# Kernel tuning notes

Hardware: AMD Instinct MI355X
Metric: run time of the kernel (lower is better)

Reference implementation:

```python
import jax, jax.numpy as jnp
import numpy as np

DIM = 1024
NUM_HEADS = 16
HEAD_DIM = DIM // NUM_HEADS
B, S, E = 4, 8192, 2000


def setup_inputs() -> dict:
    key = jax.random.key(0)
    ks = jax.random.split(key, 16)
    sd = 0.02
    inp = {
        "x": jax.random.normal(ks[0], (B, S, DIM), dtype=jnp.float32),
        "src_indices": jax.random.randint(ks[1], (E,), 0, S),
        "dst_indices": jax.random.randint(ks[2], (E,), 0, S),
        # linear weights stored [in, out] (applied as x @ W + b)
        "Wq": jax.random.normal(ks[3], (DIM, DIM), jnp.float32) * sd,
        "bq": jnp.zeros((DIM,), jnp.float32),
        "Wk": jax.random.normal(ks[4], (DIM, DIM), jnp.float32) * sd,
        "bk": jnp.zeros((DIM,), jnp.float32),
        "Wv": jax.random.normal(ks[5], (DIM, DIM), jnp.float32) * sd,
        "bv": jnp.zeros((DIM,), jnp.float32),
        "Wo": jax.random.normal(ks[6], (DIM, DIM), jnp.float32) * sd,
        "bo": jnp.zeros((DIM,), jnp.float32),
        "edge_weight": jax.random.normal(ks[7], (1, NUM_HEADS, 1), jnp.float32),
        "W1": jax.random.normal(ks[8], (2 * HEAD_DIM, HEAD_DIM), jnp.float32) * sd,
        "b1": jnp.zeros((HEAD_DIM,), jnp.float32),
        "W2": jax.random.normal(ks[9], (HEAD_DIM, 1), jnp.float32) * sd,
        "b2": jnp.zeros((1,), jnp.float32),
    }
    return inp


def reference(x, src_indices, dst_indices, Wq, bq, Wk, bk, Wv, bv, Wo, bo,
              edge_weight, W1, b1, W2, b2):
    Bs, Sl, D = x.shape
    H, hd = NUM_HEADS, HEAD_DIM
    scale = hd ** -0.5

    def heads(t):  # [B,S,D] -> [B,H,S,hd]
        return t.reshape(Bs, Sl, H, hd).transpose(0, 2, 1, 3)

    q = heads(x @ Wq + bq)
    k = heads(x @ Wk + bk)
    v = heads(x @ Wv + bv)

    q_src = jnp.take(q, src_indices, axis=2)   # [B,H,E,hd]
    k_dst = jnp.take(k, dst_indices, axis=2)   # [B,H,E,hd]
    v_dst = jnp.take(v, dst_indices, axis=2)   # [B,H,E,hd]

    ef = jnp.concatenate([q_src, k_dst], axis=-1)          # [B,H,E,2hd]
    h = jax.nn.gelu(ef @ W1 + b1, approximate=False)       # [B,H,E,hd]
    scores = (h @ W2 + b2) * scale                         # [B,H,E,1]
    attn = jax.nn.softmax(scores, axis=2)                  # softmax over all edges
    attn = attn * edge_weight[..., None]                   # [1,H,1,1] broadcast

    weighted = attn * v_dst                                # [B,H,E,hd]
    out = jnp.zeros((Bs, H, Sl, hd), x.dtype).at[:, :, src_indices, :].add(weighted)

    final = out.transpose(0, 2, 1, 3).reshape(Bs, Sl, D)
    return final @ Wo + bo
```

## Files before the change

kernel.cpp:

```cpp
#include <hip/hip_runtime.h>
#include <hip/hip_bf16.h>
#include <math.h>

#define DIMK 1024
#define NH 16
#define HD 64
#define BB 4
#define SS 8192
#define NKT 32

typedef __attribute__((ext_vector_type(8))) short bf16x8;
typedef __attribute__((ext_vector_type(8))) unsigned short ushort8;
typedef __attribute__((ext_vector_type(4))) unsigned short us4;
typedef __attribute__((ext_vector_type(4))) float f32x4;

#define MFMA16(a, b, c) __builtin_amdgcn_mfma_f32_16x16x32_bf16((a), (b), (c), 0, 0, 0)

__device__ __forceinline__ unsigned short f32_to_bf16_rne(float f) {
  unsigned int u = __float_as_uint(f);
  u = (u + 0x7fffu + ((u >> 16) & 1u)) >> 16;
  return (unsigned short)u;
}
__device__ __forceinline__ float bf16_bits_to_f32(unsigned short b) {
  return __uint_as_float(((unsigned int)b) << 16);
}
__device__ __forceinline__ void gload16(const void* g, void* l) {
  __builtin_amdgcn_global_load_lds((const __attribute__((address_space(1))) void*)g,
                                   (__attribute__((address_space(3))) void*)l, 16, 0, 0);
}

__global__ __launch_bounds__(256) void fill_out_kernel(const float4* __restrict__ bo4,
                                                       float4* __restrict__ out, int total4) {
  for (int i = blockIdx.x * 256 + threadIdx.x; i < total4; i += gridDim.x * 256)
    out[i] = bo4[i & 255];
}

__global__ __launch_bounds__(256) void prep_w2(
    const float* __restrict__ Wv, const float* __restrict__ Wo,
    unsigned short* __restrict__ Bkv, unsigned short* __restrict__ Bo) {
  const float* W = blockIdx.z ? Wo : Wv;
  unsigned short* Bpan = blockIdx.z ? Bo : Bkv;
  const int pnoff = blockIdx.z ? 0 : 8;
  __shared__ float st[64][65];
  const int bk = blockIdx.x * 64, bn = blockIdx.y * 64;
  const int t = threadIdx.x;
  const int lr = t >> 4, lc = (t & 15) * 4;
#pragma unroll
  for (int i = 0; i < 4; i++) {
    int k = lr + i * 16;
    float4 v = *(const float4*)(W + (size_t)(bk + k) * DIMK + bn + lc);
    st[k][lc] = v.x; st[k][lc + 1] = v.y; st[k][lc + 2] = v.z; st[k][lc + 3] = v.w;
  }
  __syncthreads();
  const int ktile = (bk + lc) >> 5, c = lc & 31;
#pragma unroll
  for (int i = 0; i < 4; i++) {
    const int nl = lr + i * 16;
    const int n = bn + nl;
    const int r = n & 127, pn = (n >> 7) + pnoff;
    const int q = (c >> 3) ^ ((r >> 1) & 3);
    const size_t byteoff = (size_t)r * 64 + q * 16 + (c & 7) * 2;
    us4 hv, lv;
#pragma unroll
    for (int j = 0; j < 4; j++) {
      float v = st[lc + j][nl];
      unsigned short hb = f32_to_bf16_rne(v);
      hv[j] = hb;
      lv[j] = f32_to_bf16_rne(v - bf16_bits_to_f32(hb));
    }
    char* base = (char*)Bpan;
    *(us4*)(base + (((size_t)pn * 64 + ktile) << 13) + byteoff) = hv;
    *(us4*)(base + (((size_t)pn * 64 + 32 + ktile) << 13) + byteoff) = lv;
  }
}

__global__ __launch_bounds__(256) void prep_wfold(
    const float* __restrict__ Wq, const float* __restrict__ Wk,
    const float* __restrict__ W1,
    unsigned short* __restrict__ Bq, unsigned short* __restrict__ Bkv) {
  const int which = blockIdx.z;
  const float* W = which ? Wk : Wq;
  unsigned short* Bpan = which ? Bkv : Bq;
  const int d_off = which ? 64 : 0;
  const int cc = blockIdx.x, jc = blockIdx.y;
  __shared__ float Wb[64][65];
  __shared__ float W1b[64][65];
  const int t = threadIdx.x;
  for (int idx = t; idx < 64 * 64; idx += 256) {
    int rrow = idx >> 6, dd = idx & 63;
    Wb[rrow][dd] = W[(size_t)(cc * 64 + rrow) * DIMK + jc * 64 + dd];
    W1b[rrow][dd] = W1[(size_t)(d_off + rrow) * 64 + dd];
  }
  __syncthreads();
  const int n = t & 63, g0 = t >> 6;
  const int pn = jc >> 1;
  const int r = (jc & 1) * 64 + n;
  const int sw = (r >> 1) & 3;
  char* base = (char*)Bpan;
#pragma unroll
  for (int i = 0; i < 4; ++i) {
    const int cl0 = (g0 + 4 * i) * 4;
    float a0 = 0.f, a1 = 0.f, a2 = 0.f, a3 = 0.f;
    for (int d = 0; d < 64; ++d) {
      const float w1v = W1b[d][n];
      a0 = fmaf(Wb[cl0 + 0][d], w1v, a0);
      a1 = fmaf(Wb[cl0 + 1][d], w1v, a1);
      a2 = fmaf(Wb[cl0 + 2][d], w1v, a2);
      a3 = fmaf(Wb[cl0 + 3][d], w1v, a3);
    }
    float av[4] = {a0, a1, a2, a3};
    const int c = cc * 64 + cl0;
    const int kt = c >> 5, kcol = c & 31;
    const int q = (kcol >> 3) ^ sw;
    const size_t byteoff = (size_t)r * 64 + q * 16 + (kcol & 7) * 2;
    us4 hv, lv;
#pragma unroll
    for (int j = 0; j < 4; j++) {
      unsigned short hb = f32_to_bf16_rne(av[j]);
      hv[j] = hb;
      lv[j] = f32_to_bf16_rne(av[j] - bf16_bits_to_f32(hb));
    }
    *(us4*)(base + (((size_t)pn * 64 + kt) << 13) + byteoff) = hv;
    *(us4*)(base + (((size_t)pn * 64 + 32 + kt) << 13) + byteoff) = lv;
  }
}

__global__ __launch_bounds__(256) void prep_bias(
    const float* __restrict__ bq, const float* __restrict__ bk,
    const float* __restrict__ b1, const float* __restrict__ W1,
    float* __restrict__ bqf, float* __restrict__ bkf) {
  const int j = blockIdx.x * 256 + threadIdx.x;
  const int h = j >> 6, n = j & 63;
  float sq = 0.f, sk = 0.f;
  for (int d = 0; d < 64; ++d) {
    sq = fmaf(bq[h * 64 + d], W1[d * 64 + n], sq);
    sk = fmaf(bk[h * 64 + d], W1[(64 + d) * 64 + n], sk);
  }
  bqf[j] = sq;
  bkf[j] = sk + b1[n];
}

__global__ __launch_bounds__(256) void prep_a(const float* __restrict__ X,
                                              const int* __restrict__ gidx,
                                              unsigned short* __restrict__ Apan, int M, int E) {
  const int row = blockIdx.x;
  const int r = row & 255, mt = row >> 8;
  const int c0 = threadIdx.x * 4;
  const int kt = c0 >> 5, c = c0 & 31;
  const int q = (c >> 3) ^ ((r >> 1) & 3);
  const size_t byteoff = (size_t)r * 64 + q * 16 + (c & 7) * 2;
  char* base = (char*)Apan;
  us4 hv = (us4){0, 0, 0, 0}, lv = (us4){0, 0, 0, 0};
  if (row < M) {
    const float* sr;
    if (gidx) {
      int b = row / E, e = row - b * E;
      sr = X + ((size_t)b * SS + gidx[e]) * DIMK;
    } else {
      sr = X + (size_t)row * DIMK;
    }
    float4 v = *(const float4*)(sr + c0);
    float vv[4] = {v.x, v.y, v.z, v.w};
#pragma unroll
    for (int i = 0; i < 4; i++) {
      unsigned short hb = f32_to_bf16_rne(vv[i]);
      hv[i] = hb;
      lv[i] = f32_to_bf16_rne(vv[i] - bf16_bits_to_f32(hb));
    }
  }
  *(us4*)(base + (((size_t)(mt * 64 + kt)) << 14) + byteoff) = hv;
  *(us4*)(base + (((size_t)(mt * 64 + 32 + kt)) << 14) + byteoff) = lv;
}

__global__ __launch_bounds__(1024) void first_occ(const int* __restrict__ src,
                                                  int* __restrict__ fidx,
                                                  int* __restrict__ mark, int E) {
  __shared__ int tbl[SS];
  for (int i = threadIdx.x; i < SS; i += 1024) tbl[i] = 0x7fffffff;
  __syncthreads();
  for (int e = threadIdx.x; e < E; e += 1024) atomicMin(&tbl[src[e]], e);
  __syncthreads();
  for (int e = threadIdx.x; e < E; e += 1024) mark[e] = 0;
  __syncthreads();
  for (int e = threadIdx.x; e < E; e += 1024) {
    int f = tbl[src[e]];
    fidx[e] = f;
    if (f != e) mark[f] = 1;
  }
}

template <int BM, int MODE>
__global__ __launch_bounds__(512, 2) void gemmT(
    const unsigned short* __restrict__ Apan, const unsigned short* __restrict__ Bpan,
    const float* __restrict__ bias, const float* __restrict__ bias2,
    float* __restrict__ out, int ldc, int nty,
    const int* __restrict__ fidx, const int* __restrict__ srci, int M, int E) {
  constexpr int MF = BM / 32;
  constexpr int NF = 4;
  constexpr int AT = BM * 32;
  __shared__ unsigned short ldsAh[2][AT];
  __shared__ unsigned short ldsAl[2][AT];
  __shared__ unsigned short ldsBh[2][8192];
  __shared__ unsigned short ldsBl[2][8192];

  const int tid = threadIdx.x, lane = tid & 63, wv = tid >> 6;
  const int wr = wv >> 2, wc = wv & 3;

  const int w = (blockIdx.x & 7) * ((int)gridDim.x >> 3) + ((int)blockIdx.x >> 3);
  const int mi = w / nty, nt_ = w - mi * nty;
  const int m0 = mi * BM, n0 = nt_ * 256;

  const int rr = lane & 15, lq = lane >> 4;
  const int swz = (rr >> 1) & 3;
  const int aoff = (wr * (BM / 2) + rr) * 32 + ((lq ^ swz) << 3);
  const int boff = (wc * 64 + rr) * 32 + ((lq ^ swz) << 3);

  const int pt = (BM == 256) ? mi : (mi >> 1);
  const int rowbase = (BM == 256) ? 0 : (mi & 1) * 128;
  const char* Apb = (const char*)Apan + (((size_t)pt * 64) << 14) + (size_t)rowbase * 64;
  const char* Bpb = (const char*)Bpan;
  const int stoff = wv * 1024 + lane * 16;

  f32x4 acc[MF][NF];
#pragma unroll
  for (int i = 0; i < MF; i++)
#pragma unroll
    for (int j = 0; j < NF; j++) acc[i][j] = (f32x4){0.f, 0.f, 0.f, 0.f};

  auto stage = [&](int kt, int buf) {
    const char* sAh = Apb + ((size_t)kt << 14) + stoff;
    const char* sAl = Apb + ((size_t)(32 + kt) << 14) + stoff;
    gload16(sAh, &ldsAh[buf][wv * 512]);
    gload16(sAl, &ldsAl[buf][wv * 512]);
    if (BM == 256) {
      gload16(sAh + 8192, &ldsAh[buf][wv * 512 + 4096]);
      gload16(sAl + 8192, &ldsAl[buf][wv * 512 + 4096]);
    }
    const char* sB0h = Bpb + (((size_t)(2 * nt_) * 64 + kt) << 13) + stoff;
    const char* sB1h = Bpb + (((size_t)(2 * nt_ + 1) * 64 + kt) << 13) + stoff;
    const char* sB0l = Bpb + (((size_t)(2 * nt_) * 64 + 32 + kt) << 13) + stoff;
    const char* sB1l = Bpb + (((size_t)(2 * nt_ + 1) * 64 + 32 + kt) << 13) + stoff;
    gload16(sB0h, &ldsBh[buf][wv * 512]);
    gload16(sB1h, &ldsBh[buf][wv * 512 + 4096]);
    gload16(sB0l, &ldsBl[buf][wv * 512]);
    gload16(sB1l, &ldsBl[buf][wv * 512 + 4096]);
  };

  stage(0, 0);
  asm volatile("s_waitcnt vmcnt(0)" ::: "memory");
  __builtin_amdgcn_sched_barrier(0);
  __builtin_amdgcn_s_barrier();

  for (int kt = 0; kt < NKT; ++kt) {
    const int buf = kt & 1;
    const unsigned short* Ah = ldsAh[buf];
    const unsigned short* Al = ldsAl[buf];
    const unsigned short* Bh = ldsBh[buf];
    const unsigned short* Bl = ldsBl[buf];

    bf16x8 fbh[NF], fah[MF], fal[MF], fbl[NF];
#pragma unroll
    for (int nf = 0; nf < NF; ++nf) fbh[nf] = *(const bf16x8*)(Bh + boff + nf * 512);
#pragma unroll
    for (int mf = 0; mf < MF; ++mf) fah[mf] = *(const bf16x8*)(Ah + aoff + mf * 512);
    __builtin_amdgcn_sched_barrier(0);
#pragma unroll
    for (int mf = 0; mf < MF; ++mf) fal[mf] = *(const bf16x8*)(Al + aoff + mf * 512);
    __builtin_amdgcn_sched_barrier(0);
#pragma unroll
    for (int nf = 0; nf < NF; ++nf) fbl[nf] = *(const bf16x8*)(Bl + boff + nf * 512);
    __builtin_amdgcn_sched_barrier(0);

    if (kt + 1 < NKT) stage(kt + 1, buf ^ 1);

    asm volatile("s_waitcnt lgkmcnt(%0)" ::"i"(MF + NF) : "memory");
    __builtin_amdgcn_sched_barrier(0);
    __builtin_amdgcn_s_setprio(1);
#pragma unroll
    for (int mf = 0; mf < MF; ++mf)
#pragma unroll
      for (int nf = 0; nf < NF; ++nf) acc[mf][nf] = MFMA16(fah[mf], fbh[nf], acc[mf][nf]);
    __builtin_amdgcn_s_setprio(0);

    asm volatile("s_waitcnt lgkmcnt(%0)" ::"i"(NF) : "memory");
    __builtin_amdgcn_sched_barrier(0);
    __builtin_amdgcn_s_setprio(1);
#pragma unroll
    for (int mf = 0; mf < MF; ++mf)
#pragma unroll
      for (int nf = 0; nf < NF; ++nf) acc[mf][nf] = MFMA16(fal[mf], fbh[nf], acc[mf][nf]);
    __builtin_amdgcn_s_setprio(0);

    asm volatile("s_waitcnt lgkmcnt(0)" ::: "memory");
    if (kt + 1 < NKT) {
      asm volatile("s_waitcnt vmcnt(0)" ::: "memory");
      __builtin_amdgcn_sched_barrier(0);
      __builtin_amdgcn_s_barrier();
    } else {
      __builtin_amdgcn_sched_barrier(0);
    }

    __builtin_amdgcn_s_setprio(1);
#pragma unroll
    for (int mf = 0; mf < MF; ++mf)
#pragma unroll
      for (int nf = 0; nf < NF; ++nf) acc[mf][nf] = MFMA16(fah[mf], fbl[nf], acc[mf][nf]);
    __builtin_amdgcn_s_setprio(0);
  }

  const int cq = lane >> 4, cr = lane & 15;
#pragma unroll
  for (int nf = 0; nf < NF; ++nf) {
    const int col = n0 + wc * 64 + nf * 16 + cr;
    const float bv = (MODE == 0 && bias2 != nullptr && col >= DIMK) ? bias2[col - DIMK]
                                                                    : bias[col & (DIMK - 1)];
#pragma unroll
    for (int mf = 0; mf < MF; ++mf) {
#pragma unroll
      for (int r = 0; r < 4; ++r) {
        const int mrow = m0 + wr * (BM / 2) + mf * 16 + cq * 4 + r;
        if (mrow >= M) continue;
        if (MODE == 0) {
          out[(size_t)mrow * ldc + col] = acc[mf][nf][r] + bv;
        } else {
          int b = mrow / E, e = mrow - b * E;
          if (fidx[e] == e) {
            int orow = b * SS + srci[e];
            out[(size_t)orow * ldc + col] = acc[mf][nf][r] + bv;
          }
        }
      }
    }
  }
}

__global__ __launch_bounds__(256) void edge_scores_f(
    const float* __restrict__ hq, const float* __restrict__ hk,
    const float* __restrict__ W2, const float* __restrict__ b2,
    float* __restrict__ scores, int E, int CH) {
  const int tid = threadIdx.x, lane = tid & 63, w = tid >> 6;
  const int bh = blockIdx.x / CH, ch = blockIdx.x - bh * CH;
  const int b = bh >> 4, h = bh & 15;
  const float w2 = W2[lane];
  const float b2v = b2[0];
#pragma unroll
  for (int i = 0; i < 8; ++i) {
    const int e = ch * 32 + w * 8 + i;
    if (e >= E) break;
    const size_t row = (size_t)(b * E + e);
    float hv = hq[row * 1024 + h * 64 + lane] + hk[row * 2048 + h * 64 + lane];
    hv = 0.5f * hv * (1.f + erff(hv * 0.70710678118654752f));
    float p = hv * w2;
#pragma unroll
    for (int off = 32; off; off >>= 1) p += __shfl_xor(p, off, 64);
    if (lane == 0) scores[(size_t)(b * NH + h) * E + e] = (p + b2v) * 0.125f;
  }
}

__global__ __launch_bounds__(256) void softmax_ew(float* __restrict__ scores,
                                                  const float* __restrict__ ew, int E) {
  const int row = blockIdx.x;
  const int h = row & (NH - 1);
  float* s = scores + (size_t)row * E;
  const int tid = threadIdx.x, lane = tid & 63, w = tid >> 6;
  __shared__ float red[4];

  float vals[8];
  float mx = -1e30f;
#pragma unroll
  for (int i = 0; i < 8; i++) {
    int j = tid + i * 256;
    vals[i] = (j < E) ? s[j] : -1e30f;
    mx = fmaxf(mx, vals[i]);
  }
#pragma unroll
  for (int off = 32; off; off >>= 1) mx = fmaxf(mx, __shfl_xor(mx, off, 64));
  if (lane == 0) red[w] = mx;
  __syncthreads();
  mx = fmaxf(fmaxf(red[0], red[1]), fmaxf(red[2], red[3]));
  __syncthreads();

  float sum = 0.f;
#pragma unroll
  for (int i = 0; i < 8; i++) {
    vals[i] = __expf(vals[i] - mx);
    if (tid + i * 256 < E) sum += vals[i];
  }
#pragma unroll
  for (int off = 32; off; off >>= 1) sum += __shfl_xor(sum, off, 64);
  if (lane == 0) red[w] = sum;
  __syncthreads();
  sum = red[0] + red[1] + red[2] + red[3];

  const float scaleout = ew[h] / sum;
#pragma unroll
  for (int i = 0; i < 8; i++) {
    int j = tid + i * 256;
    if (j < E) s[j] = vals[i] * scaleout;
  }
}

__global__ __launch_bounds__(256) void weight_split(
    const float* __restrict__ vd, int ldv, const float* __restrict__ attn,
    float* __restrict__ wrow, unsigned short* __restrict__ Apan, int M, int E) {
  const int row = blockIdx.x;
  const int r = row & 255, mt = row >> 8;
  const int c0 = threadIdx.x * 4;
  const int kt = c0 >> 5, c = c0 & 31;
  const int q = (c >> 3) ^ ((r >> 1) & 3);
  const size_t byteoff = (size_t)r * 64 + q * 16 + (c & 7) * 2;
  char* base = (char*)Apan;
  us4 hv = (us4){0, 0, 0, 0}, lv = (us4){0, 0, 0, 0};
  if (row < M) {
    const int b = row / E, e = row - b * E;
    const float a = attn[(size_t)(b * NH + (c0 >> 6)) * E + e];
    float4 v = *(const float4*)(vd + (size_t)row * ldv + c0);
    v.x *= a; v.y *= a; v.z *= a; v.w *= a;
    *(float4*)(wrow + (size_t)row * DIMK + c0) = v;
    float vv[4] = {v.x, v.y, v.z, v.w};
#pragma unroll
    for (int i = 0; i < 4; i++) {
      unsigned short hb = f32_to_bf16_rne(vv[i]);
      hv[i] = hb;
      lv[i] = f32_to_bf16_rne(vv[i] - bf16_bits_to_f32(hb));
    }
  }
  *(us4*)(base + (((size_t)(mt * 64 + kt)) << 14) + byteoff) = hv;
  *(us4*)(base + (((size_t)(mt * 64 + 32 + kt)) << 14) + byteoff) = lv;
}

__global__ __launch_bounds__(256) void dup_add(const int* __restrict__ f,
                                               float* __restrict__ wrow, int E) {
  const int e = blockIdx.x;
  const int fe = f[e];
  if (fe == e) return;
  const int d = threadIdx.x * 4;
#pragma unroll
  for (int b = 0; b < BB; b++) {
    const float4 v = *(const float4*)(wrow + (size_t)(b * E + e) * DIMK + d);
    float* dst = wrow + (size_t)(b * E + fe) * DIMK + d;
    atomicAdd(dst + 0, v.x);
    atomicAdd(dst + 1, v.y);
    atomicAdd(dst + 2, v.z);
    atomicAdd(dst + 3, v.w);
  }
}

__global__ __launch_bounds__(256) void dup_fix(const int* __restrict__ fidx,
                                               const int* __restrict__ mark,
                                               const float* __restrict__ wrow,
                                               unsigned short* __restrict__ Apan, int E) {
  const int e = blockIdx.x;
  if (fidx[e] != e || !mark[e]) return;
  const int c0 = threadIdx.x * 4;
  const int kt = c0 >> 5, c = c0 & 31;
  char* base = (char*)Apan;
  for (int b = 0; b < BB; b++) {
    const int row = b * E + e;
    const int r = row & 255, mt = row >> 8;
    const int q = (c >> 3) ^ ((r >> 1) & 3);
    const size_t byteoff = (size_t)r * 64 + q * 16 + (c & 7) * 2;
    float4 v = *(const float4*)(wrow + (size_t)row * DIMK + c0);
    float vv[4] = {v.x, v.y, v.z, v.w};
    us4 hv, lv;
#pragma unroll
    for (int i = 0; i < 4; i++) {
      unsigned short hb = f32_to_bf16_rne(vv[i]);
      hv[i] = hb;
      lv[i] = f32_to_bf16_rne(vv[i] - bf16_bits_to_f32(hb));
    }
    *(us4*)(base + (((size_t)(mt * 64 + kt)) << 14) + byteoff) = hv;
    *(us4*)(base + (((size_t)(mt * 64 + 32 + kt)) << 14) + byteoff) = lv;
  }
}

extern "C" void kernel_launch(void* const* d_in, const int* in_sizes, int n_in,
                              void* d_out, int out_size, void* d_ws, size_t ws_size,
                              hipStream_t stream) {
  const float* x = (const float*)d_in[0];
  const int* src = (const int*)d_in[1];
  const int* dst = (const int*)d_in[2];
  const float* Wq = (const float*)d_in[3];
  const float* bq = (const float*)d_in[4];
  const float* Wk = (const float*)d_in[5];
  const float* bk = (const float*)d_in[6];
  const float* Wv = (const float*)d_in[7];
  const float* bv = (const float*)d_in[8];
  const float* Wo = (const float*)d_in[9];
  const float* bo = (const float*)d_in[10];
  const float* ew = (const float*)d_in[11];
  const float* W1 = (const float*)d_in[12];
  const float* b1 = (const float*)d_in[13];
  const float* W2 = (const float*)d_in[14];
  const float* b2 = (const float*)d_in[15];
  float* out = (float*)d_out;

  const int E = in_sizes[1];
  const int M = BB * E;
  const int gx = (M + 255) / 256;
  const int Mpad = gx * 256;
  const int mi128 = gx * 2;

  char* w = (char*)d_ws;
  float* qs = (float*)w; w += (size_t)M * DIMK * 4;
  float* kv = (float*)w; w += (size_t)M * 2048 * 4;
  float* sc = (float*)w; w += (size_t)BB * NH * E * 4;
  int* fidx = (int*)w; w += (((size_t)E * 4) + 255) & ~(size_t)255;
  int* mark = (int*)w; w += (((size_t)E * 4) + 255) & ~(size_t)255;
  float* bqf = (float*)w; w += 1024 * 4;
  float* bkf = (float*)w; w += 1024 * 4;
  unsigned short* Bq = (unsigned short*)w; w += (size_t)8 * 64 * 8192;
  unsigned short* Bkv = (unsigned short*)w; w += (size_t)16 * 64 * 8192;
  unsigned short* Bo = (unsigned short*)w; w += (size_t)8 * 64 * 8192;
  unsigned short* Apan = (unsigned short*)w; w += (size_t)gx * 64 * 16384;

  float* wrow = qs;

  const int total4 = BB * SS * (DIMK / 4);
  fill_out_kernel<<<2048, 256, 0, stream>>>((const float4*)bo, (float4*)out, total4);

  prep_w2<<<dim3(16, 16, 2), 256, 0, stream>>>(Wv, Wo, Bkv, Bo);
  prep_wfold<<<dim3(16, 16, 2), 256, 0, stream>>>(Wq, Wk, W1, Bq, Bkv);
  prep_bias<<<4, 256, 0, stream>>>(bq, bk, b1, W1, bqf, bkf);

  first_occ<<<1, 1024, 0, stream>>>(src, fidx, mark, E);

  prep_a<<<Mpad, 256, 0, stream>>>(x, src, Apan, M, E);
  gemmT<128, 0><<<mi128 * 4, 512, 0, stream>>>(Apan, Bq, bqf, nullptr, qs, DIMK, 4,
                                               nullptr, nullptr, M, E);

  prep_a<<<Mpad, 256, 0, stream>>>(x, dst, Apan, M, E);
  gemmT<256, 0><<<gx * 8, 512, 0, stream>>>(Apan, Bkv, bkf, bv, kv, 2048, 8,
                                            nullptr, nullptr, M, E);

  const int CH = (E + 31) / 32;
  edge_scores_f<<<BB * NH * CH, 256, 0, stream>>>(qs, kv, W2, b2, sc, E, CH);
  softmax_ew<<<BB * NH, 256, 0, stream>>>(sc, ew, E);

  weight_split<<<Mpad, 256, 0, stream>>>(kv + 1024, 2048, sc, wrow, Apan, M, E);
  dup_add<<<E, 256, 0, stream>>>(fidx, wrow, E);
  dup_fix<<<E, 256, 0, stream>>>(fidx, mark, wrow, Apan, E);

  gemmT<128, 1><<<mi128 * 4, 512, 0, stream>>>(Apan, Bo, bo, nullptr, out, DIMK, 4,
                                               fidx, src, M, E);
}
```

Baseline: 334.2 us.

## Add 256x256-tile split-bf16 GEMM with 4 waves for K/V projection

Adds a dedicated gemmW kernel that computes the fused K/V projection with 256-thread blocks, each wave holding an 8x8 grid of 16x16 MFMA accumulators. It double-buffers LDS and interleaves staged waits with the three hi/lo bf16 MFMA passes. Each wave now covers a larger output tile, so fragment reuse per LDS read goes up and LDS traffic per flop goes down. The cost is heavy register pressure (256 accumulator floats plus fragments) and one block per CU, which could cause spills or poor latency hiding.

```diff
diff --git a/kernel.cpp b/kernel.cpp
--- a/kernel.cpp
+++ b/kernel.cpp
@@ -186,6 +186,140 @@
     int f = tbl[src[e]];
     fidx[e] = f;
     if (f != e) mark[f] = 1;
+  }
+}
+
+__global__ __launch_bounds__(256, 1) void gemmW(
+    const unsigned short* __restrict__ Apan, const unsigned short* __restrict__ Bpan,
+    const float* __restrict__ bias, const float* __restrict__ bias2,
+    float* __restrict__ out, int ldc, int nty, int M, int E) {
+  __shared__ unsigned short ldsAh[2][8192];
+  __shared__ unsigned short ldsAl[2][8192];
+  __shared__ unsigned short ldsBh[2][8192];
+  __shared__ unsigned short ldsBl[2][8192];
+
+  const int tid = threadIdx.x, lane = tid & 63, wv = tid >> 6;
+  const int wr = wv >> 1, wc = wv & 1;
+
+  const int w = (blockIdx.x & 7) * ((int)gridDim.x >> 3) + ((int)blockIdx.x >> 3);
+  const int mi = w / nty, nt_ = w - mi * nty;
+  const int m0 = mi * 256, n0 = nt_ * 256;
+
+  const int rr = lane & 15, lq = lane >> 4;
+  const int swz = (rr >> 1) & 3;
+  const int aoff = wr * 4096 + rr * 32 + ((lq ^ swz) << 3);
+  const int boff = wc * 4096 + rr * 32 + ((lq ^ swz) << 3);
+
+  const char* Apb = (const char*)Apan + (((size_t)mi * 64) << 14);
+  const char* Bpb = (const char*)Bpan;
+  const int soff = (wv * 64 + lane) * 16;
+
+  f32x4 acc[8][8];
+#pragma unroll
+  for (int i = 0; i < 8; i++)
+#pragma unroll
+    for (int j = 0; j < 8; j++) acc[i][j] = (f32x4){0.f, 0.f, 0.f, 0.f};
+
+  auto stage = [&](int kt, int buf) {
+    const char* sAh = Apb + ((size_t)kt << 14);
+    const char* sAl = Apb + ((size_t)(32 + kt) << 14);
+#pragma unroll
+    for (int s = 0; s < 4; ++s) {
+      const int o = soff + s * 4096;
+      gload16(sAh + o, &ldsAh[buf][o >> 1]);
+      gload16(sAl + o, &ldsAl[buf][o >> 1]);
+    }
+    const char* sB0h = Bpb + (((size_t)(2 * nt_) * 64 + kt) << 13);
+    const char* sB1h = Bpb + (((size_t)(2 * nt_ + 1) * 64 + kt) << 13);
+    const char* sB0l = Bpb + (((size_t)(2 * nt_) * 64 + 32 + kt) << 13);
+    const char* sB1l = Bpb + (((size_t)(2 * nt_ + 1) * 64 + 32 + kt) << 13);
+#pragma unroll
+    for (int s = 0; s < 2; ++s) {
+      const int o = soff + s * 4096;
+      gload16(sB0h + o, &ldsBh[buf][o >> 1]);
+      gload16(sB1h + o, &ldsBh[buf][4096 + (o >> 1)]);
+      gload16(sB0l + o, &ldsBl[buf][o >> 1]);
+      gload16(sB1l + o, &ldsBl[buf][4096 + (o >> 1)]);
+    }
+  };
+
+  stage(0, 0);
+  asm volatile("s_waitcnt vmcnt(0)" ::: "memory");
+  __builtin_amdgcn_sched_barrier(0);
+  __builtin_amdgcn_s_barrier();
+
+  for (int kt = 0; kt < NKT; ++kt) {
+    const int buf = kt & 1;
+    const unsigned short* Ah = ldsAh[buf];
+    const unsigned short* Al = ldsAl[buf];
+    const unsigned short* Bh = ldsBh[buf];
+    const unsigned short* Bl = ldsBl[buf];
+
+    bf16x8 fbh[8], fah[8], fal[8], fbl[8];
+#pragma unroll
+    for (int nf = 0; nf < 8; ++nf) fbh[nf] = *(const bf16x8*)(Bh + boff + nf * 512);
+#pragma unroll
+    for (int mf = 0; mf < 8; ++mf) fah[mf] = *(const bf16x8*)(Ah + aoff + mf * 512);
+    __builtin_amdgcn_sched_barrier(0);
+#pragma unroll
+    for (int mf = 0; mf < 8; ++mf) fal[mf] = *(const bf16x8*)(Al + aoff + mf * 512);
+    __builtin_amdgcn_sched_barrier(0);
+#pragma unroll
+    for (int nf = 0; nf < 8; ++nf) fbl[nf] = *(const bf16x8*)(Bl + boff + nf * 512);
+    __builtin_amdgcn_sched_barrier(0);
+
+    if (kt + 1 < NKT) stage(kt + 1, buf ^ 1);
+
+    asm volatile("s_waitcnt lgkmcnt(15)" ::: "memory");
+    __builtin_amdgcn_sched_barrier(0);
+    __builtin_amdgcn_s_setprio(1);
+#pragma unroll
+    for (int mf = 0; mf < 8; ++mf)
+#pragma unroll
+      for (int nf = 0; nf < 8; ++nf) acc[mf][nf] = MFMA16(fah[mf], fbh[nf], acc[mf][nf]);
+    __builtin_amdgcn_s_setprio(0);
+
+    asm volatile("s_waitcnt lgkmcnt(8)" ::: "memory");
+    __builtin_amdgcn_sched_barrier(0);
+    __builtin_amdgcn_s_setprio(1);
+#pragma unroll
+    for (int mf = 0; mf < 8; ++mf)
+#pragma unroll
+      for (int nf = 0; nf < 8; ++nf) acc[mf][nf] = MFMA16(fal[mf], fbh[nf], acc[mf][nf]);
+    __builtin_amdgcn_s_setprio(0);
+
+    asm volatile("s_waitcnt lgkmcnt(0)" ::: "memory");
+    if (kt + 1 < NKT) {
+      asm volatile("s_waitcnt vmcnt(0)" ::: "memory");
+      __builtin_amdgcn_sched_barrier(0);
+      __builtin_amdgcn_s_barrier();
+    } else {
+      __builtin_amdgcn_sched_barrier(0);
+    }
+
+    __builtin_amdgcn_s_setprio(1);
+#pragma unroll
+    for (int mf = 0; mf < 8; ++mf)
+#pragma unroll
+      for (int nf = 0; nf < 8; ++nf) acc[mf][nf] = MFMA16(fah[mf], fbl[nf], acc[mf][nf]);
+    __builtin_amdgcn_s_setprio(0);
+  }
+
+  const int cq = lane >> 4, cr = lane & 15;
+#pragma unroll
+  for (int nf = 0; nf < 8; ++nf) {
+    const int col = n0 + wc * 128 + nf * 16 + cr;
+    const float bv = (bias2 != nullptr && col >= DIMK) ? bias2[col - DIMK]
+                                                       : bias[col & (DIMK - 1)];
+#pragma unroll
+    for (int mf = 0; mf < 8; ++mf) {
+#pragma unroll
+      for (int r = 0; r < 4; ++r) {
+        const int mrow = m0 + wr * 128 + mf * 16 + cq * 4 + r;
+        if (mrow >= M) continue;
+        out[(size_t)mrow * ldc + col] = acc[mf][nf][r] + bv;
+      }
+    }
   }
 }
 
@@ -530,8 +664,7 @@
                                                nullptr, nullptr, M, E);
 
   prep_a<<<Mpad, 256, 0, stream>>>(x, dst, Apan, M, E);
-  gemmT<256, 0><<<gx * 8, 512, 0, stream>>>(Apan, Bkv, bkf, bv, kv, 2048, 8,
-                                            nullptr, nullptr, M, E);
+  gemmW<<<gx * 8, 256, 0, stream>>>(Apan, Bkv, bkf, bv, kv, 2048, 8, M, E);
 
   const int CH = (E + 31) / 32;
   edge_scores_f<<<BB * NH * CH, 256, 0, stream>>>(qs, kv, W2, b2, sc, E, CH);
```

New measurement: 391.4 us. 1.17x slower.
